# Optimization experiments

Hardware: AMD Instinct MI355X
Metric: run time of the kernel (lower is better)

Reference implementation:

```python
import jax, jax.numpy as jnp
import numpy as np

N, E, D, L = 50000, 800000, 128, 3  # nodes, edges, feature dim, num GraphConv layers


def setup_inputs() -> dict:
    key = jax.random.key(0)
    ks = jax.random.split(key, 6)
    x = jax.random.normal(ks[0], (N, D), dtype=jnp.float32)
    edge_index = jax.random.randint(ks[1], (2, E), 0, N, dtype=jnp.int64)
    edge_weight = jax.random.uniform(ks[2], (E,), dtype=jnp.float32)
    s = 1.0 / np.sqrt(D)  # PyG Linear default (kaiming-ish uniform bound)
    W_rel = jax.random.uniform(ks[3], (L, D, D), dtype=jnp.float32, minval=-s, maxval=s)
    b_rel = jax.random.uniform(ks[4], (L, D), dtype=jnp.float32, minval=-s, maxval=s)
    W_root = jax.random.uniform(ks[5], (L, D, D), dtype=jnp.float32, minval=-s, maxval=s)
    return {"x": x, "edge_index": edge_index, "edge_weight": edge_weight,
            "W_rel": W_rel, "b_rel": b_rel, "W_root": W_root}


def reference(x, edge_index, edge_weight, W_rel, b_rel, W_root):
    # PyG GraphConv: out = lin_rel(sum_{j->i} e_ji * x_j) + lin_root(x_i)
    src, dst = edge_index[0], edge_index[1]

    def conv(h, i):
        msg = h[src] * edge_weight[:, None]                     # [E, D] gather + per-edge scale
        agg = jax.ops.segment_sum(msg, dst, num_segments=N)     # [N, D] scatter-add
        return agg @ W_rel[i] + b_rel[i] + h @ W_root[i]

    h = x
    for i in range(L - 1):
        h = jax.nn.relu(conv(h, i))  # dropout is identity at inference
    return conv(h, L - 1)
```

## Files before the change

### kernel.cpp

```cpp
#include <hip/hip_runtime.h>

#define D 128
#define SC_IT 16

typedef __attribute__((ext_vector_type(8))) short bf16x8;
typedef __attribute__((ext_vector_type(4))) float f32x4;

__device__ __forceinline__ float uif(unsigned u) { return __uint_as_float(u); }
__device__ __forceinline__ unsigned short f2bf(float f) {
    unsigned u = __float_as_uint(f);
    u += 0x7fffu + ((u >> 16) & 1u);
    return (unsigned short)(u >> 16);
}
__device__ __forceinline__ float bf2f(unsigned short h) {
    return __uint_as_float(((unsigned)h) << 16);
}

__global__ __launch_bounds__(256) void hist_kernel(
    const int* __restrict__ dst, int* __restrict__ counts, int E)
{
    int e = blockIdx.x * 256 + threadIdx.x;
    if (e < E) atomicAdd(&counts[dst[e]], 1);
}

__global__ __launch_bounds__(256) void blocksum_kernel(
    const int* __restrict__ counts, int* __restrict__ bsums, int N)
{
    __shared__ int red[256];
    int t = threadIdx.x;
    int i = blockIdx.x * 256 + t;
    red[t] = (i < N) ? counts[i] : 0;
    __syncthreads();
    #pragma unroll
    for (int off = 128; off > 0; off >>= 1) {
        if (t < off) red[t] += red[t + off];
        __syncthreads();
    }
    if (t == 0) bsums[blockIdx.x] = red[0];
}

__global__ __launch_bounds__(256) void scansums_kernel(
    int* __restrict__ bsums, int nb)
{
    __shared__ int s[256];
    int t = threadIdx.x;
    int v = (t < nb) ? bsums[t] : 0;
    s[t] = v;
    __syncthreads();
    #pragma unroll
    for (int off = 1; off < 256; off <<= 1) {
        int tmp = (t >= off) ? s[t - off] : 0;
        __syncthreads();
        s[t] += tmp;
        __syncthreads();
    }
    if (t < nb) bsums[t] = s[t] - v;
}

__global__ __launch_bounds__(256) void emit_kernel(
    const int* __restrict__ counts, const int* __restrict__ bsums,
    int* __restrict__ row_ptr, int* __restrict__ cursor, int N, int E)
{
    __shared__ int s[256];
    int t = threadIdx.x;
    int i = blockIdx.x * 256 + t;
    int v = (i < N) ? counts[i] : 0;
    s[t] = v;
    __syncthreads();
    #pragma unroll
    for (int off = 1; off < 256; off <<= 1) {
        int tmp = (t >= off) ? s[t - off] : 0;
        __syncthreads();
        s[t] += tmp;
        __syncthreads();
    }
    int excl = s[t] - v + bsums[blockIdx.x];
    if (i < N) { row_ptr[i] = excl; cursor[i] = excl; }
    if (blockIdx.x == 0 && t == 0) row_ptr[N] = E;
}

__global__ __launch_bounds__(256) void scatter_xcd_kernel(
    const int* __restrict__ src, const int* __restrict__ dst,
    const float* __restrict__ ew, int* __restrict__ cursor,
    int2* __restrict__ edata, int E, int N)
{
    int xcd   = blockIdx.x & 7;
    int chunk = blockIdx.x >> 3;
    int lo = (int)(((long long)xcd * N) >> 3);
    int hi = (int)(((long long)(xcd + 1) * N) >> 3);
    int base = chunk * (256 * SC_IT) + threadIdx.x;
    #pragma unroll
    for (int it = 0; it < SC_IT; ++it) {
        int e = base + it * 256;
        if (e < E) {
            int d = __builtin_nontemporal_load(&dst[e]);
            if (d >= lo && d < hi) {
                int pos = atomicAdd(&cursor[d], 1);
                int s = __builtin_nontemporal_load(&src[e]);
                float w = __builtin_nontemporal_load(&ew[e]);
                edata[pos] = make_int2(s, __float_as_int(w));
            }
        }
    }
}

__global__ __launch_bounds__(256) void convert_x_kernel(
    const float* __restrict__ x, short* __restrict__ Ah, int N)
{
    int t = blockIdx.x * 256 + threadIdx.x;
    if (t >= N * 64) return;
    int row = t >> 6;
    int c2  = (t & 63) * 2;
    float2 v = *(const float2*)(x + (size_t)row * D + c2);
    *(unsigned*)(Ah + (size_t)row * D + c2) =
        ((unsigned)f2bf(v.y) << 16) | f2bf(v.x);
}

__global__ __launch_bounds__(256) void convert_w_kernel(
    const float* __restrict__ Wrel, const float* __restrict__ Wroot,
    short* __restrict__ WhiT, short* __restrict__ WloT, int total)
{
    int t = blockIdx.x * 256 + threadIdx.x;
    if (t >= total) return;
    int l = t >> 15;
    int rem = t & 32767;
    int k = rem >> 7;
    int c = rem & 127;
    float f = (k < 128) ? Wrel[(size_t)l * 16384 + k * D + c]
                        : Wroot[(size_t)l * 16384 + (k - 128) * D + c];
    unsigned short h = f2bf(f);
    WhiT[(size_t)l * 32768 + c * 256 + k] = (short)h;
    WloT[(size_t)l * 32768 + c * 256 + k] = (short)f2bf(f - bf2f(h));
}

__global__ __launch_bounds__(256) void gather_bf16(
    const short* __restrict__ Ah, short* __restrict__ aggHi,
    short* __restrict__ aggLo,
    const int2* __restrict__ edata, const int* __restrict__ row_ptr, int N)
{
    int wave = (blockIdx.x * 256 + threadIdx.x) >> 6;
    int lane = threadIdx.x & 63;
    if (wave >= N) return;
    int g   = lane >> 4;
    int l16 = lane & 15;
    int beg = row_ptr[wave];
    int cnt = row_ptr[wave + 1] - beg;

    const short* hbase = Ah + l16 * 8;

    float acc[8];
    #pragma unroll
    for (int c = 0; c < 8; ++c) acc[c] = 0.f;

    for (int base = 0; base < cnt; base += 64) {
        int k = base + lane;
        int2 ed = make_int2(0, 0);
        if (k < cnt) ed = edata[beg + k];
        int m = min(64, cnt - base);
        for (int j = 0; j < m; j += 16) {
            int   sA = __shfl(ed.x, j + g);      float wA = __shfl(uif(ed.y), j + g);
            int   sB = __shfl(ed.x, j + 4 + g);  float wB = __shfl(uif(ed.y), j + 4 + g);
            int   sC = __shfl(ed.x, j + 8 + g);  float wC = __shfl(uif(ed.y), j + 8 + g);
            int   sD = __shfl(ed.x, j + 12 + g); float wD = __shfl(uif(ed.y), j + 12 + g);
            bf16x8 rA = *(const bf16x8*)(hbase + (size_t)sA * D);
            bf16x8 rB = *(const bf16x8*)(hbase + (size_t)sB * D);
            bf16x8 rC = *(const bf16x8*)(hbase + (size_t)sC * D);
            bf16x8 rD = *(const bf16x8*)(hbase + (size_t)sD * D);
            #pragma unroll
            for (int c = 0; c < 8; ++c)
                acc[c] = fmaf(wA, bf2f((unsigned short)rA[c]), acc[c]);
            #pragma unroll
            for (int c = 0; c < 8; ++c)
                acc[c] = fmaf(wB, bf2f((unsigned short)rB[c]), acc[c]);
            #pragma unroll
            for (int c = 0; c < 8; ++c)
                acc[c] = fmaf(wC, bf2f((unsigned short)rC[c]), acc[c]);
            #pragma unroll
            for (int c = 0; c < 8; ++c)
                acc[c] = fmaf(wD, bf2f((unsigned short)rD[c]), acc[c]);
        }
    }

    #pragma unroll
    for (int c = 0; c < 8; ++c) {
        acc[c] += __shfl_xor(acc[c], 16);
        acc[c] += __shfl_xor(acc[c], 32);
    }

    if (g < 2) {
        bf16x8 pk;
        #pragma unroll
        for (int c = 0; c < 8; ++c) {
            unsigned short h = f2bf(acc[c]);
            pk[c] = (g == 0) ? (short)h : (short)f2bf(acc[c] - bf2f(h));
        }
        short* dstp = (g == 0 ? aggHi : aggLo) + (size_t)wave * D + l16 * 8;
        *(bf16x8*)dstp = pk;
    }
}

#define STAGE_W(WSRC)                                                           \
    _Pragma("unroll")                                                           \
    for (int r = 0; r < 16; ++r) {                                              \
        int u = r * 256 + tid;                                                  \
        bf16x8 v = *(const bf16x8*)((WSRC) + (size_t)u * 8);                    \
        int scol = u >> 5, sku = u & 31;                                        \
        *(bf16x8*)((char*)bsh + scol * 512 + ((sku ^ (scol & 7)) << 4)) = v;    \
    }

#define MFMA_SEG(APTR, KUOFF)                                                   \
    _Pragma("unroll")                                                           \
    for (int ks = 0; ks < 4; ++ks) {                                            \
        bf16x8 a0 = *(const bf16x8*)((APTR) + aoff0 + ks * 32 + l4 * 8);        \
        bf16x8 a1 = *(const bf16x8*)((APTR) + aoff1 + ks * 32 + l4 * 8);        \
        _Pragma("unroll")                                                       \
        for (int n = 0; n < 4; ++n) {                                           \
            int col = wc * 64 + n * 16 + l15;                                   \
            int ku = (KUOFF) + ks * 4 + l4;                                     \
            bf16x8 b = *(const bf16x8*)((const char*)bsh + col * 512            \
                                        + ((ku ^ (col & 7)) << 4));             \
            acc0[n] = __builtin_amdgcn_mfma_f32_16x16x32_bf16(a0, b, acc0[n], 0, 0, 0); \
            acc1[n] = __builtin_amdgcn_mfma_f32_16x16x32_bf16(a1, b, acc1[n], 0, 0, 0); \
        }                                                                       \
    }

__global__ __launch_bounds__(256, 2) void gemm_mfma(
    const short* __restrict__ aggHi, const short* __restrict__ aggLo,
    const short* __restrict__ Ah, short* __restrict__ AhN,
    const short* __restrict__ WhiT, const short* __restrict__ WloT,
    const float* __restrict__ bias, float* __restrict__ outf,
    int N, int relu, int writef)
{
    __shared__ short bsh[32768];
    int tid = threadIdx.x;
    int lane = tid & 63;
    int wid = tid >> 6;
    int wr = wid >> 1, wc = wid & 1;
    int l15 = lane & 15, l4 = lane >> 4;
    int row0 = blockIdx.x * 64;

    size_t aoff0 = (size_t)(row0 + wr * 32 + l15) * D;
    size_t aoff1 = aoff0 + 16 * D;

    f32x4 acc0[4], acc1[4];
    #pragma unroll
    for (int n = 0; n < 4; ++n) {
        acc0[n] = (f32x4){0.f, 0.f, 0.f, 0.f};
        acc1[n] = (f32x4){0.f, 0.f, 0.f, 0.f};
    }

    STAGE_W(WhiT);
    __syncthreads();
    MFMA_SEG(aggHi, 0);
    MFMA_SEG(aggLo, 0);
    MFMA_SEG(Ah, 16);
    __syncthreads();
    STAGE_W(WloT);
    __syncthreads();
    MFMA_SEG(aggHi, 0);
    MFMA_SEG(Ah, 16);

    #pragma unroll
    for (int n = 0; n < 4; ++n) {
        int col = wc * 64 + n * 16 + l15;
        float bv = bias[col];
        #pragma unroll
        for (int m = 0; m < 2; ++m) {
            f32x4 a = (m == 0) ? acc0[n] : acc1[n];
            #pragma unroll
            for (int r = 0; r < 4; ++r) {
                int row = row0 + wr * 32 + m * 16 + l4 * 4 + r;
                if (row < N) {
                    float v = a[r] + bv;
                    if (relu) v = fmaxf(v, 0.f);
                    if (writef) outf[(size_t)row * D + col] = v;
                    else        AhN[(size_t)row * D + col] = (short)f2bf(v);
                }
            }
        }
    }
}

extern "C" void kernel_launch(void* const* d_in, const int* in_sizes, int n_in,
                              void* d_out, int out_size, void* d_ws, size_t ws_size,
                              hipStream_t stream)
{
    const float* x     = (const float*)d_in[0];
    const int*   ei    = (const int*)d_in[1];
    const float* ew    = (const float*)d_in[2];
    const float* Wrel  = (const float*)d_in[3];
    const float* brel  = (const float*)d_in[4];
    const float* Wroot = (const float*)d_in[5];
    float* out = (float*)d_out;

    int N = in_sizes[0] / D;
    int E = in_sizes[2];
    int L = in_sizes[3] / (D * D);
    int Npad = ((N + 63) / 64) * 64;
    const int* src = ei;
    const int* dst = ei + E;
    int nb = (N + 255) / 256;

    short* Ah0   = (short*)d_ws;
    short* Ah1   = Ah0 + (size_t)Npad * D;
    short* aggHi = Ah1 + (size_t)Npad * D;
    short* aggLo = aggHi + (size_t)Npad * D;
    short* WhiT  = aggLo + (size_t)Npad * D;
    short* WloT  = WhiT + (size_t)L * 32768;
    int2*  edata   = (int2*)(WloT + (size_t)L * 32768);
    int*   row_ptr = (int*)(edata + E);
    int*   cursor  = row_ptr + (N + 1);
    int*   counts  = cursor + N;
    int*   bsums   = counts + N;

    dim3 blk256(256);
    dim3 grdE((E + 255) / 256);
    dim3 grdN(nb);
    int nchunks = (E + 256 * SC_IT - 1) / (256 * SC_IT);
    dim3 grdScat(nchunks * 8);
    dim3 grdGather((N * 64 + 255) / 256);
    dim3 grdGemm(Npad / 64);
    dim3 grdCX((N * 64 + 255) / 256);
    dim3 grdCW((L * 32768 + 255) / 256);

    hipMemsetAsync(counts, 0, (size_t)N * sizeof(int), stream);
    hist_kernel<<<grdE, blk256, 0, stream>>>(dst, counts, E);
    blocksum_kernel<<<grdN, blk256, 0, stream>>>(counts, bsums, N);
    scansums_kernel<<<1, blk256, 0, stream>>>(bsums, nb);
    emit_kernel<<<grdN, blk256, 0, stream>>>(counts, bsums, row_ptr, cursor, N, E);
    scatter_xcd_kernel<<<grdScat, blk256, 0, stream>>>(src, dst, ew, cursor, edata, E, N);

    convert_w_kernel<<<grdCW, blk256, 0, stream>>>(Wrel, Wroot, WhiT, WloT, L * 32768);
    convert_x_kernel<<<grdCX, blk256, 0, stream>>>(x, Ah0, N);

    for (int l = 0; l < L; ++l) {
        const short* Ain  = (l & 1) ? Ah1 : Ah0;
        short*       Aout = (l & 1) ? Ah0 : Ah1;
        gather_bf16<<<grdGather, blk256, 0, stream>>>(Ain, aggHi, aggLo, edata, row_ptr, N);
        gemm_mfma<<<grdGemm, blk256, 0, stream>>>(
            aggHi, aggLo, Ain, Aout, WhiT + (size_t)l * 32768, WloT + (size_t)l * 32768,
            brel + (size_t)l * D, out, N, (l < L - 1) ? 1 : 0, (l == L - 1) ? 1 : 0);
    }
}
```

Measured before the change: 295.7 us.

## Pack edge src and bf16 weight into 32 bits; vectorize hist and scatter loads

Edge records shrink from an int2 (int src, fp32 weight) to one 32-bit word: a 16-bit source index plus the weight rounded to bf16. This halves edge-list traffic in the gather and lets one shuffle per edge replace two. The histogram and scatter kernels now load destinations with 128-bit vector loads, several edges per thread. The 16-bit index only works when N is at most 65536 (here N=50000), and rounding the weights to bf16 loses precision.

```diff
diff --git a/kernel.cpp b/kernel.cpp
--- a/kernel.cpp
+++ b/kernel.cpp
@@ -5,6 +5,7 @@
 
 typedef __attribute__((ext_vector_type(8))) short bf16x8;
 typedef __attribute__((ext_vector_type(4))) float f32x4;
+typedef __attribute__((ext_vector_type(4))) int   int4v;
 
 __device__ __forceinline__ float uif(unsigned u) { return __uint_as_float(u); }
 __device__ __forceinline__ unsigned short f2bf(float f) {
@@ -19,8 +20,17 @@
 __global__ __launch_bounds__(256) void hist_kernel(
     const int* __restrict__ dst, int* __restrict__ counts, int E)
 {
-    int e = blockIdx.x * 256 + threadIdx.x;
-    if (e < E) atomicAdd(&counts[dst[e]], 1);
+    int base = (blockIdx.x * 256 + threadIdx.x) * 4;
+    if (base >= E) return;
+    if (base + 4 <= E) {
+        int4v d = *(const int4v*)(dst + base);
+        atomicAdd(&counts[d.x], 1);
+        atomicAdd(&counts[d.y], 1);
+        atomicAdd(&counts[d.z], 1);
+        atomicAdd(&counts[d.w], 1);
+    } else {
+        for (int e = base; e < E; ++e) atomicAdd(&counts[dst[e]], 1);
+    }
 }
 
 __global__ __launch_bounds__(256) void blocksum_kernel(
@@ -79,27 +89,45 @@
     if (blockIdx.x == 0 && t == 0) row_ptr[N] = E;
 }
 
+#define SC_CLAIM(DV, IT)                                                        \
+    do {                                                                        \
+        int d_ = (DV);                                                          \
+        if (d_ >= lo && d_ < hi) {                                              \
+            int e_ = base + (IT);                                               \
+            int pos_ = atomicAdd(&cursor[d_], 1);                               \
+            unsigned pk_ = (unsigned)(unsigned short)                           \
+                               __builtin_nontemporal_load(&src[e_])             \
+                         | ((unsigned)f2bf(                                     \
+                               __builtin_nontemporal_load(&ew[e_])) << 16);     \
+            edata[pos_] = pk_;                                                  \
+        }                                                                       \
+    } while (0)
+
 __global__ __launch_bounds__(256) void scatter_xcd_kernel(
     const int* __restrict__ src, const int* __restrict__ dst,
     const float* __restrict__ ew, int* __restrict__ cursor,
-    int2* __restrict__ edata, int E, int N)
+    unsigned* __restrict__ edata, int E, int N)
 {
     int xcd   = blockIdx.x & 7;
     int chunk = blockIdx.x >> 3;
     int lo = (int)(((long long)xcd * N) >> 3);
     int hi = (int)(((long long)(xcd + 1) * N) >> 3);
-    int base = chunk * (256 * SC_IT) + threadIdx.x;
-    #pragma unroll
-    for (int it = 0; it < SC_IT; ++it) {
-        int e = base + it * 256;
-        if (e < E) {
-            int d = __builtin_nontemporal_load(&dst[e]);
-            if (d >= lo && d < hi) {
-                int pos = atomicAdd(&cursor[d], 1);
-                int s = __builtin_nontemporal_load(&src[e]);
-                float w = __builtin_nontemporal_load(&ew[e]);
-                edata[pos] = make_int2(s, __float_as_int(w));
-            }
+    int base = (chunk * 256 + threadIdx.x) * SC_IT;
+    if (base >= E) return;
+    if (base + SC_IT <= E) {
+        const int4v* dp = (const int4v*)(dst + base);
+        int4v d0 = __builtin_nontemporal_load(dp + 0);
+        int4v d1 = __builtin_nontemporal_load(dp + 1);
+        int4v d2 = __builtin_nontemporal_load(dp + 2);
+        int4v d3 = __builtin_nontemporal_load(dp + 3);
+        SC_CLAIM(d0.x,  0); SC_CLAIM(d0.y,  1); SC_CLAIM(d0.z,  2); SC_CLAIM(d0.w,  3);
+        SC_CLAIM(d1.x,  4); SC_CLAIM(d1.y,  5); SC_CLAIM(d1.z,  6); SC_CLAIM(d1.w,  7);
+        SC_CLAIM(d2.x,  8); SC_CLAIM(d2.y,  9); SC_CLAIM(d2.z, 10); SC_CLAIM(d2.w, 11);
+        SC_CLAIM(d3.x, 12); SC_CLAIM(d3.y, 13); SC_CLAIM(d3.z, 14); SC_CLAIM(d3.w, 15);
+    } else {
+        for (int it = 0; it < SC_IT; ++it) {
+            int e = base + it;
+            if (e < E) SC_CLAIM(dst[e], it);
         }
     }
 }
@@ -136,7 +164,7 @@
 __global__ __launch_bounds__(256) void gather_bf16(
     const short* __restrict__ Ah, short* __restrict__ aggHi,
     short* __restrict__ aggLo,
-    const int2* __restrict__ edata, const int* __restrict__ row_ptr, int N)
+    const unsigned* __restrict__ edata, const int* __restrict__ row_ptr, int N)
 {
     int wave = (blockIdx.x * 256 + threadIdx.x) >> 6;
     int lane = threadIdx.x & 63;
@@ -154,18 +182,22 @@
 
     for (int base = 0; base < cnt; base += 64) {
         int k = base + lane;
-        int2 ed = make_int2(0, 0);
-        if (k < cnt) ed = edata[beg + k];
+        int ed = 0;
+        if (k < cnt) ed = (int)edata[beg + k];
         int m = min(64, cnt - base);
         for (int j = 0; j < m; j += 16) {
-            int   sA = __shfl(ed.x, j + g);      float wA = __shfl(uif(ed.y), j + g);
-            int   sB = __shfl(ed.x, j + 4 + g);  float wB = __shfl(uif(ed.y), j + 4 + g);
-            int   sC = __shfl(ed.x, j + 8 + g);  float wC = __shfl(uif(ed.y), j + 8 + g);
-            int   sD = __shfl(ed.x, j + 12 + g); float wD = __shfl(uif(ed.y), j + 12 + g);
-            bf16x8 rA = *(const bf16x8*)(hbase + (size_t)sA * D);
-            bf16x8 rB = *(const bf16x8*)(hbase + (size_t)sB * D);
-            bf16x8 rC = *(const bf16x8*)(hbase + (size_t)sC * D);
-            bf16x8 rD = *(const bf16x8*)(hbase + (size_t)sD * D);
+            int eA = __shfl(ed, j + g);
+            int eB = __shfl(ed, j + 4 + g);
+            int eC = __shfl(ed, j + 8 + g);
+            int eD = __shfl(ed, j + 12 + g);
+            float wA = uif((unsigned)eA & 0xffff0000u);
+            float wB = uif((unsigned)eB & 0xffff0000u);
+            float wC = uif((unsigned)eC & 0xffff0000u);
+            float wD = uif((unsigned)eD & 0xffff0000u);
+            bf16x8 rA = *(const bf16x8*)(hbase + (size_t)(eA & 0xffff) * D);
+            bf16x8 rB = *(const bf16x8*)(hbase + (size_t)(eB & 0xffff) * D);
+            bf16x8 rC = *(const bf16x8*)(hbase + (size_t)(eC & 0xffff) * D);
+            bf16x8 rD = *(const bf16x8*)(hbase + (size_t)(eD & 0xffff) * D);
             #pragma unroll
             for (int c = 0; c < 8; ++c)
                 acc[c] = fmaf(wA, bf2f((unsigned short)rA[c]), acc[c]);
@@ -307,14 +339,14 @@
     short* aggLo = aggHi + (size_t)Npad * D;
     short* WhiT  = aggLo + (size_t)Npad * D;
     short* WloT  = WhiT + (size_t)L * 32768;
-    int2*  edata   = (int2*)(WloT + (size_t)L * 32768);
+    unsigned* edata = (unsigned*)(WloT + (size_t)L * 32768);
     int*   row_ptr = (int*)(edata + E);
     int*   cursor  = row_ptr + (N + 1);
     int*   counts  = cursor + N;
     int*   bsums   = counts + N;
 
     dim3 blk256(256);
-    dim3 grdE((E + 255) / 256);
+    dim3 grdH((E + 1023) / 1024);
     dim3 grdN(nb);
     int nchunks = (E + 256 * SC_IT - 1) / (256 * SC_IT);
     dim3 grdScat(nchunks * 8);
@@ -324,7 +356,7 @@
     dim3 grdCW((L * 32768 + 255) / 256);
 
     hipMemsetAsync(counts, 0, (size_t)N * sizeof(int), stream);
-    hist_kernel<<<grdE, blk256, 0, stream>>>(dst, counts, E);
+    hist_kernel<<<grdH, blk256, 0, stream>>>(dst, counts, E);
     blocksum_kernel<<<grdN, blk256, 0, stream>>>(counts, bsums, N);
     scansums_kernel<<<1, blk256, 0, stream>>>(bsums, nb);
     emit_kernel<<<grdN, blk256, 0, stream>>>(counts, bsums, row_ptr, cursor, N, E);
```

After: 307.8 us. +4.1%, slower.
